# Optimization experiments

Hardware: AMD Instinct MI355X
Metric: run time of the kernel (lower is better)

The kernel has to match this reference:

```python
import jax, jax.numpy as jnp
import numpy as np
import math

B, N, DEG, D = 128, 512, 8, 128
E = B * N * DEG
K1 = math.ceil(0.8 * N)    # 410 nodes kept per graph after pool1
K2 = math.ceil(0.8 * K1)   # 328 nodes kept per graph after pool2


def setup_inputs() -> dict:
    key = jax.random.key(0)
    ks = jax.random.split(key, 24)
    x = jax.random.normal(ks[0], (B * N, D), jnp.float32)
    # random edges within each graph, then offset to global node ids
    src_l = jax.random.randint(ks[1], (B, N * DEG), 0, N)
    dst_l = jax.random.randint(ks[2], (B, N * DEG), 0, N)
    offs = (jnp.arange(B) * N)[:, None]
    edge_index = jnp.stack([(src_l + offs).reshape(-1), (dst_l + offs).reshape(-1)]).astype(jnp.int32)
    w = lambda k, s: (jax.random.normal(k, s, jnp.float32) * 0.05)
    return {
        "x": x, "edge_index": edge_index,
        "W1r": w(ks[3], (D, 128)), "W1n": w(ks[4], (D, 128)), "b1": jnp.zeros((128,), jnp.float32),
        "p1": w(ks[5], (128,)),
        "W2r": w(ks[6], (128, 128)), "W2n": w(ks[7], (128, 128)), "b2": jnp.zeros((128,), jnp.float32),
        "p2": w(ks[8], (128,)),
        "lw1": w(ks[9], (256, 128)), "lb1": jnp.zeros((128,), jnp.float32),
        "lw2": w(ks[10], (128, 64)), "lb2": jnp.zeros((64,), jnp.float32),
        "lw3": w(ks[11], (64, 1)), "lb3": jnp.zeros((1,), jnp.float32),
    }


def _conv(h, src, dst, Wr, Wn, b):
    # GraphConv-style spatio-temporal message passing, sum aggregation
    msg = h[src] @ Wn                                   # [E, 128]
    agg = jax.ops.segment_sum(msg, dst, num_segments=B * N)
    return h @ Wr + agg + b


def _topk_mask(score, k, prev_mask):
    # per-graph top-k node selection (TopKPooling); restrict to prev_mask
    s = jnp.where(prev_mask, score, -jnp.inf).reshape(B, N)
    idx = jax.lax.top_k(s, k)[1]                        # [B, k]
    m = jnp.zeros((B, N), bool).at[jnp.arange(B)[:, None], idx].set(True)
    return m.reshape(B * N)


def _readout(h, mask, k):
    # concat of global max pool and global mean pool over kept nodes
    hm = jnp.where(mask[:, None], h, -jnp.inf).reshape(B, N, -1)
    gmax = hm.max(axis=1)
    gmean = (h * mask[:, None].astype(h.dtype)).reshape(B, N, -1).sum(axis=1) / k
    return jnp.concatenate([gmax, gmean], axis=1)       # [B, 256]


def reference(x, edge_index, W1r, W1n, b1, p1, W2r, W2n, b2, p2, lw1, lb1, lw2, lb2, lw3, lb3):
    src, dst = edge_index[0], edge_index[1]
    # conv1 + relu
    h = jax.nn.relu(_conv(x, src, dst, W1r, W1n, b1))
    # pool1: score = h.p/||p||, keep top-K1, gate by tanh(score)
    s1 = h @ p1 / jnp.linalg.norm(p1)
    m1 = _topk_mask(s1, K1, jnp.ones(B * N, bool))
    h = h * (jnp.tanh(s1) * m1.astype(h.dtype))[:, None]
    x1 = _readout(h, m1, K1)
    # conv2 + relu (dropped nodes have zero features -> zero messages)
    h = jax.nn.relu(_conv(h, src, dst, W2r, W2n, b2))
    s2 = h @ p2 / jnp.linalg.norm(p2)
    m2 = _topk_mask(s2, K2, m1)
    h = h * (jnp.tanh(s2) * m2.astype(h.dtype))[:, None]
    x2 = _readout(h, m2, K2)
    # MLP head (bn1/bn2 are defined but unused in the original forward; dropout is eval-mode identity)
    z = x1 + x2
    z = jax.nn.relu(z @ lw1 + lb1)
    z = jax.nn.relu(z @ lw2 + lb2)
    return jax.nn.sigmoid(z @ lw3 + lb3).squeeze(-1)    # [B]
```

## Files before the change

### kernel.cpp

```cpp
#include <hip/hip_runtime.h>
#include <math.h>

constexpr int B = 128;
constexpr int N = 512;
constexpr int DEG = 8;
constexpr int D = 128;
constexpr int E = B * N * DEG;
constexpr int EPG = N * DEG;
constexpr int NN = B * N;
constexpr int K1 = 410;
constexpr int K2 = 328;
constexpr int PADDEG = 16;

typedef __attribute__((ext_vector_type(8))) short short8;
typedef __attribute__((ext_vector_type(4))) float f32x4;

__device__ __forceinline__ unsigned short f2bf(float f) {
    unsigned int u = __float_as_uint(f);
    unsigned int r = (u + 0x7fffu + ((u >> 16) & 1u)) >> 16;
    return (unsigned short)r;
}
__device__ __forceinline__ float bf2f(unsigned short h) {
    return __uint_as_float(((unsigned int)h) << 16);
}

__global__ __launch_bounds__(256) void k_prepw(const float* __restrict__ W0,
                                               const float* __restrict__ W1,
                                               const float* __restrict__ W2,
                                               const float* __restrict__ W3,
                                               unsigned short* __restrict__ wt) {
    const float* Ws[4] = {W0, W1, W2, W3};
    const int m = blockIdx.x;
    const float* src = Ws[m];
    unsigned short* dH = wt + (size_t)m * 32768;
    unsigned short* dL = dH + 16384;
    for (int idx = threadIdx.x; idx < 16384; idx += 256) {
        int kk = idx >> 7, n = idx & 127;
        float v = src[idx];
        unsigned short h = f2bf(v);
        unsigned short l = f2bf(v - bf2f(h));
        dH[n * 128 + kk] = h;
        dL[n * 128 + kk] = l;
    }
}

__global__ __launch_bounds__(512) void k_csr2(const int* __restrict__ ei,
                                              int* __restrict__ coff,
                                              int* __restrict__ ccnt,
                                              int* __restrict__ csrc,
                                              int* __restrict__ csrcp) {
    __shared__ int cnt[512];
    __shared__ int sa[512];
    __shared__ int offs[512];
    __shared__ int cur[512];
    const int g = blockIdx.x, t = threadIdx.x;
    const int base = g * N;
    const int* srcs = ei + g * EPG;
    const int* dsts = ei + E + g * EPG;
    {
        const int n = base + t;
        int4 self = make_int4(n, n, n, n);
        #pragma unroll
        for (int k4 = 0; k4 < PADDEG / 4; ++k4)
            *(int4*)&csrcp[(size_t)n * PADDEG + k4 * 4] = self;
    }
    cnt[t] = 0;
    __syncthreads();
    #pragma unroll
    for (int e = t; e < EPG; e += 512)
        atomicAdd(&cnt[dsts[e] - base], 1);
    __syncthreads();
    int v = cnt[t];
    sa[t] = v;
    __syncthreads();
    for (int d = 1; d < 512; d <<= 1) {
        int add = (t >= d) ? sa[t - d] : 0;
        __syncthreads();
        sa[t] += add;
        __syncthreads();
    }
    const int excl = sa[t] - v;
    offs[t] = excl;
    cur[t] = excl;
    coff[base + t] = g * EPG + excl;
    ccnt[base + t] = v;
    __syncthreads();
    #pragma unroll
    for (int e = t; e < EPG; e += 512) {
        int d = dsts[e] - base;
        int pos = atomicAdd(&cur[d], 1);
        int s = srcs[e];
        csrc[g * EPG + pos] = s;
        int lpos = pos - offs[d];
        if (lpos < PADDEG) csrcp[(size_t)(base + d) * PADDEG + lpos] = s;
    }
}

__global__ __launch_bounds__(256, 2) void k_gather(const float* __restrict__ feat,
                                                   const float* __restrict__ gate,
                                                   const int* __restrict__ coff,
                                                   const int* __restrict__ ccnt,
                                                   const int* __restrict__ csrc,
                                                   const int* __restrict__ csrcp,
                                                   float* __restrict__ aggout) {
    const int bid = blockIdx.x;
    const int xcd = bid & 7;
    const int j = bid >> 3;
    const int g = ((j & 15) << 3) | xcd;
    const int chunk = j >> 4;
    const int t = threadIdx.x;
    const int lane = t & 31, grp = t >> 5;
    const int fo = lane * 4;
    #pragma unroll
    for (int it = 0; it < 4; ++it) {
        const int n = g * N + chunk * 32 + it * 8 + grp;
        const int deg = ccnt[n];
        int idx[PADDEG];
        *(int4*)&idx[0]  = *(const int4*)&csrcp[(size_t)n * PADDEG + 0];
        *(int4*)&idx[4]  = *(const int4*)&csrcp[(size_t)n * PADDEG + 4];
        *(int4*)&idx[8]  = *(const int4*)&csrcp[(size_t)n * PADDEG + 8];
        *(int4*)&idx[12] = *(const int4*)&csrcp[(size_t)n * PADDEG + 12];
        float4 acc = make_float4(0.f, 0.f, 0.f, 0.f);
        #pragma unroll
        for (int k = 0; k < PADDEG; ++k) {
            if (k < deg) {
                float wk = gate ? gate[idx[k]] : 1.0f;
                float4 v = *(const float4*)&feat[(size_t)idx[k] * D + fo];
                acc.x = fmaf(v.x, wk, acc.x);
                acc.y = fmaf(v.y, wk, acc.y);
                acc.z = fmaf(v.z, wk, acc.z);
                acc.w = fmaf(v.w, wk, acc.w);
            }
        }
        if (deg > PADDEG) {
            const int start = coff[n];
            for (int k = PADDEG; k < deg; ++k) {
                int ix = csrc[start + k];
                float gt = gate ? gate[ix] : 1.0f;
                float4 v = *(const float4*)&feat[(size_t)ix * D + fo];
                acc.x = fmaf(v.x, gt, acc.x);
                acc.y = fmaf(v.y, gt, acc.y);
                acc.z = fmaf(v.z, gt, acc.z);
                acc.w = fmaf(v.w, gt, acc.w);
            }
        }
        *(float4*)&aggout[(size_t)n * D + fo] = acc;
    }
}

__global__ __launch_bounds__(256, 2) void k_gemm(const float* __restrict__ A0,
                                                 const float* __restrict__ gateA,
                                                 const float* __restrict__ A1,
                                                 const unsigned short* __restrict__ W0t,
                                                 const unsigned short* __restrict__ W1t,
                                                 const float* __restrict__ bias,
                                                 const float* __restrict__ pvec,
                                                 float* __restrict__ out,
                                                 float* __restrict__ sun) {
    __shared__ unsigned short AsH[128 * 40], AsL[128 * 40];
    __shared__ unsigned short BsH[128 * 40], BsL[128 * 40];
    __shared__ float red[128 * 33];
    const int t = threadIdx.x;
    const int r0 = blockIdx.x * 128;
    const int w = t >> 6, lane = t & 63;
    const int lr = lane & 15, kg = (lane >> 4) * 8;
    const int wm = (w >> 1) * 64, wn = (w & 1) * 64;
    const int arow = t >> 1, kb = (t & 1) * 16;
    const float ga = gateA ? gateA[r0 + arow] : 1.0f;

    f32x4 acc[4][4];
    #pragma unroll
    for (int mt = 0; mt < 4; ++mt)
        #pragma unroll
        for (int nt = 0; nt < 4; ++nt)
            acc[mt][nt] = (f32x4)(0.f);

    for (int phase = 0; phase < 2; ++phase) {
        const float* Ap = phase ? A1 : A0;
        const unsigned short* WH = phase ? W1t : W0t;
        const unsigned short* WL = WH + 16384;
        const float gmul = phase ? 1.0f : ga;
        for (int c = 0; c < 4; ++c) {
            const int k0 = c * 32;
            __syncthreads();
            #pragma unroll
            for (int i = 0; i < 4; ++i) {
                float4 av = *(const float4*)&Ap[(size_t)(r0 + arow) * D + k0 + kb + i * 4];
                av.x *= gmul; av.y *= gmul; av.z *= gmul; av.w *= gmul;
                unsigned int h0 = f2bf(av.x), h1 = f2bf(av.y), h2 = f2bf(av.z), h3 = f2bf(av.w);
                uint2 ph; ph.x = h0 | (h1 << 16); ph.y = h2 | (h3 << 16);
                *(uint2*)&AsH[arow * 40 + kb + i * 4] = ph;
                unsigned int l0 = f2bf(av.x - bf2f(h0)), l1 = f2bf(av.y - bf2f(h1));
                unsigned int l2 = f2bf(av.z - bf2f(h2)), l3 = f2bf(av.w - bf2f(h3));
                uint2 pl; pl.x = l0 | (l1 << 16); pl.y = l2 | (l3 << 16);
                *(uint2*)&AsL[arow * 40 + kb + i * 4] = pl;
            }
            {
                const int part = t & 3;
                #pragma unroll
                for (int rep = 0; rep < 2; ++rep) {
                    const int n = (t >> 2) + rep * 64;
                    *(int4*)&BsH[n * 40 + part * 8] = *(const int4*)&WH[n * 128 + k0 + part * 8];
                    *(int4*)&BsL[n * 40 + part * 8] = *(const int4*)&WL[n * 128 + k0 + part * 8];
                }
            }
            __syncthreads();
            short8 aH[4], aL[4], bH[4], bL[4];
            #pragma unroll
            for (int mt = 0; mt < 4; ++mt) {
                aH[mt] = *(const short8*)&AsH[(wm + mt * 16 + lr) * 40 + kg];
                aL[mt] = *(const short8*)&AsL[(wm + mt * 16 + lr) * 40 + kg];
            }
            #pragma unroll
            for (int nt = 0; nt < 4; ++nt) {
                bH[nt] = *(const short8*)&BsH[(wn + nt * 16 + lr) * 40 + kg];
                bL[nt] = *(const short8*)&BsL[(wn + nt * 16 + lr) * 40 + kg];
            }
            #pragma unroll
            for (int mt = 0; mt < 4; ++mt)
                #pragma unroll
                for (int nt = 0; nt < 4; ++nt) {
                    acc[mt][nt] = __builtin_amdgcn_mfma_f32_16x16x32_bf16(aH[mt], bH[nt], acc[mt][nt], 0, 0, 0);
                    acc[mt][nt] = __builtin_amdgcn_mfma_f32_16x16x32_bf16(aH[mt], bL[nt], acc[mt][nt], 0, 0, 0);
                    acc[mt][nt] = __builtin_amdgcn_mfma_f32_16x16x32_bf16(aL[mt], bH[nt], acc[mt][nt], 0, 0, 0);
                }
        }
    }
    float bb[4], pv[4];
    #pragma unroll
    for (int nt = 0; nt < 4; ++nt) {
        bb[nt] = bias[wn + nt * 16 + lr];
        pv[nt] = pvec[wn + nt * 16 + lr];
    }
    #pragma unroll
    for (int mt = 0; mt < 4; ++mt) {
        #pragma unroll
        for (int r = 0; r < 4; ++r) {
            const int rowl = wm + mt * 16 + (lane >> 4) * 4 + r;
            const int row = r0 + rowl;
            float part = 0.f;
            #pragma unroll
            for (int nt = 0; nt < 4; ++nt) {
                float v = acc[mt][nt][r] + bb[nt];
                v = fmaxf(v, 0.f);
                out[(size_t)row * D + wn + nt * 16 + lr] = v;
                part = fmaf(v, pv[nt], part);
            }
            red[rowl * 33 + (w & 1) * 16 + lr] = part;
        }
    }
    __syncthreads();
    if (t < 128) {
        float s = 0.f;
        #pragma unroll
        for (int j = 0; j < 32; ++j) s += red[t * 33 + j];
        sun[r0 + t] = s;
    }
}

__global__ __launch_bounds__(1024) void k_topk_readout(const float* __restrict__ sun,
                                                       const float* __restrict__ p,
                                                       const float* __restrict__ prevmask,
                                                       int K, float invK,
                                                       const float* __restrict__ h,
                                                       float* __restrict__ gate,
                                                       float* __restrict__ mask,
                                                       float* __restrict__ xout) {
    __shared__ float ls[512];
    __shared__ float lg[512];
    __shared__ float lm[512];
    __shared__ float red[128];
    __shared__ float smax[16][64];
    __shared__ float ssum[16][64];
    __shared__ float norm_s;
    const int bid = blockIdx.x;
    const int g = bid >> 1, half = bid & 1;
    const int t = threadIdx.x;
    if (t < 512) {
        const int n = g * N + t;
        float s = sun[n];
        if (prevmask && prevmask[n] == 0.0f) s = -INFINITY;
        ls[t] = s;
    }
    if (t < 128) { float pvv = p[t]; red[t] = pvv * pvv; }
    __syncthreads();
    if (t < 64) red[t] += red[t + 64];
    __syncthreads();
    if (t < 32) red[t] += red[t + 32];
    __syncthreads();
    if (t == 0) {
        float s = 0.f;
        #pragma unroll
        for (int i = 0; i < 32; ++i) s += red[i];
        norm_s = sqrtf(s);
    }
    __syncthreads();
    if (t < 512) {
        const float s = ls[t];
        int cnt = 0;
        for (int jj = 0; jj < 512; ++jj) {
            float sj = ls[jj];
            cnt += (sj > s || (sj == s && jj < t)) ? 1 : 0;
        }
        const bool keep = cnt < K;
        const float gv = keep ? tanhf(s / norm_s) : 0.0f;
        const float mv = keep ? 1.0f : 0.0f;
        lg[t] = gv; lm[t] = mv;
        gate[g * N + t] = gv; mask[g * N + t] = mv;
    }
    __syncthreads();
    const int f = half * 64 + (t & 63), sub = t >> 6;
    float vmax = -INFINITY, vsum = 0.f;
    for (int nl = sub; nl < N; nl += 16) {
        const float v = h[(size_t)(g * N + nl) * D + f] * lg[nl];
        vsum += v;
        if (lm[nl] != 0.f) vmax = fmaxf(vmax, v);
    }
    smax[sub][t & 63] = vmax;
    ssum[sub][t & 63] = vsum;
    __syncthreads();
    if (t < 64) {
        float m = smax[0][t], s = ssum[0][t];
        #pragma unroll
        for (int k = 1; k < 16; ++k) { m = fmaxf(m, smax[k][t]); s += ssum[k][t]; }
        xout[g * 256 + half * 64 + t] = m;
        xout[g * 256 + 128 + half * 64 + t] = s * invK;
    }
}

__global__ __launch_bounds__(128) void k_mlp(const float* __restrict__ X1,
                                             const float* __restrict__ X2,
                                             const float* __restrict__ lw1,
                                             const float* __restrict__ lb1,
                                             const float* __restrict__ lw2,
                                             const float* __restrict__ lb2,
                                             const float* __restrict__ lw3,
                                             const float* __restrict__ lb3,
                                             float* __restrict__ out) {
    __shared__ float z[256];
    __shared__ float o1[128];
    __shared__ float o2p[64];
    const int g = blockIdx.x, t = threadIdx.x;
    z[t] = X1[g * 256 + t] + X2[g * 256 + t];
    z[t + 128] = X1[g * 256 + 128 + t] + X2[g * 256 + 128 + t];
    __syncthreads();
    float a = lb1[t];
    for (int i = 0; i < 256; ++i) a = fmaf(z[i], lw1[i * 128 + t], a);
    o1[t] = fmaxf(a, 0.f);
    __syncthreads();
    if (t < 64) {
        float b = lb2[t];
        for (int i = 0; i < 128; ++i) b = fmaf(o1[i], lw2[i * 64 + t], b);
        o2p[t] = fmaxf(b, 0.f) * lw3[t];
    }
    __syncthreads();
    if (t == 0) {
        float sacc = lb3[0];
        for (int i = 0; i < 64; ++i) sacc += o2p[i];
        out[g] = 1.f / (1.f + expf(-sacc));
    }
}

extern "C" void kernel_launch(void* const* d_in, const int* in_sizes, int n_in,
                              void* d_out, int out_size, void* d_ws, size_t ws_size,
                              hipStream_t stream) {
    const float* x    = (const float*)d_in[0];
    const int*   ei   = (const int*)d_in[1];
    const float* W1r  = (const float*)d_in[2];
    const float* W1n  = (const float*)d_in[3];
    const float* b1   = (const float*)d_in[4];
    const float* p1   = (const float*)d_in[5];
    const float* W2r  = (const float*)d_in[6];
    const float* W2n  = (const float*)d_in[7];
    const float* b2   = (const float*)d_in[8];
    const float* p2   = (const float*)d_in[9];
    const float* lw1  = (const float*)d_in[10];
    const float* lb1  = (const float*)d_in[11];
    const float* lw2  = (const float*)d_in[12];
    const float* lb2  = (const float*)d_in[13];
    const float* lw3  = (const float*)d_in[14];
    const float* lb3  = (const float*)d_in[15];
    float* out = (float*)d_out;

    char* w = (char*)d_ws;
    float* h1  = (float*)w; w += (size_t)NN * D * 4;
    float* h2  = (float*)w; w += (size_t)NN * D * 4;
    float* agg = (float*)w; w += (size_t)NN * D * 4;
    int* coff  = (int*)w;   w += (size_t)NN * 4;
    int* ccnt  = (int*)w;   w += (size_t)NN * 4;
    int* csrc  = (int*)w;   w += (size_t)E * 4;
    int* csrcp = (int*)w;   w += (size_t)NN * PADDEG * 4;
    unsigned short* wt = (unsigned short*)w; w += (size_t)4 * 2 * 16384 * 2;
    float* sun = (float*)w; w += (size_t)NN * 4;
    float* g1  = (float*)w; w += (size_t)NN * 4;
    float* m1  = (float*)w; w += (size_t)NN * 4;
    float* g2  = (float*)w; w += (size_t)NN * 4;
    float* m2  = (float*)w; w += (size_t)NN * 4;
    float* X1  = (float*)w; w += (size_t)B * 256 * 4;
    float* X2  = (float*)w; w += (size_t)B * 256 * 4;

    const unsigned short* wt1r = wt;
    const unsigned short* wt1n = wt + 1 * 32768;
    const unsigned short* wt2r = wt + 2 * 32768;
    const unsigned short* wt2n = wt + 3 * 32768;

    k_prepw<<<4, 256, 0, stream>>>(W1r, W1n, W2r, W2n, wt);
    k_csr2<<<B, 512, 0, stream>>>(ei, coff, ccnt, csrc, csrcp);

    k_gather<<<2048, 256, 0, stream>>>(x, nullptr, coff, ccnt, csrc, csrcp, agg);
    k_gemm<<<NN / 128, 256, 0, stream>>>(x, nullptr, agg, wt1r, wt1n, b1, p1, h1, sun);
    k_topk_readout<<<2 * B, 1024, 0, stream>>>(sun, p1, nullptr, K1, 1.0f / (float)K1, h1, g1, m1, X1);

    k_gather<<<2048, 256, 0, stream>>>(h1, g1, coff, ccnt, csrc, csrcp, agg);
    k_gemm<<<NN / 128, 256, 0, stream>>>(h1, g1, agg, wt2r, wt2n, b2, p2, h2, sun);
    k_topk_readout<<<2 * B, 1024, 0, stream>>>(sun, p2, m1, K2, 1.0f / (float)K2, h2, g2, m2, X2);

    k_mlp<<<B, 128, 0, stream>>>(X1, X2, lw1, lb1, lw2, lb2, lw3, lb3, out);
}
```

Before: 300.5 us.

## Fuse neighbor gather into conv GEMM A-tile load and parallelize weight prep

Removes the separate gather kernel and its aggregated-feature buffer: the GEMM now computes the neighbor sum on the fly while staging the second-phase A tile, with block-to-graph mapping chosen to keep a graph's features on one XCD. This avoids writing and re-reading an NN x 128 fp32 intermediate twice per forward. The cost is that the gather now runs with only 512 blocks, one thread per row handling 16 columns, so per-thread latency and register pressure (idx, wk and vals arrays) grow. Weight prep is also spread from 4 blocks to 256 blocks.

```diff
diff --git a/kernel.cpp b/kernel.cpp
--- a/kernel.cpp
+++ b/kernel.cpp
@@ -30,18 +30,17 @@
                                                const float* __restrict__ W3,
                                                unsigned short* __restrict__ wt) {
     const float* Ws[4] = {W0, W1, W2, W3};
-    const int m = blockIdx.x;
+    const int m = blockIdx.x >> 6;
+    const int idx = (blockIdx.x & 63) * 256 + threadIdx.x;
     const float* src = Ws[m];
     unsigned short* dH = wt + (size_t)m * 32768;
     unsigned short* dL = dH + 16384;
-    for (int idx = threadIdx.x; idx < 16384; idx += 256) {
-        int kk = idx >> 7, n = idx & 127;
-        float v = src[idx];
-        unsigned short h = f2bf(v);
-        unsigned short l = f2bf(v - bf2f(h));
-        dH[n * 128 + kk] = h;
-        dL[n * 128 + kk] = l;
-    }
+    int kk = idx >> 7, n = idx & 127;
+    float v = src[idx];
+    unsigned short h = f2bf(v);
+    unsigned short l = f2bf(v - bf2f(h));
+    dH[n * 128 + kk] = h;
+    dL[n * 128 + kk] = l;
 }
 
 __global__ __launch_bounds__(512) void k_csr2(const int* __restrict__ ei,
@@ -96,77 +95,44 @@
     }
 }
 
-__global__ __launch_bounds__(256, 2) void k_gather(const float* __restrict__ feat,
-                                                   const float* __restrict__ gate,
-                                                   const int* __restrict__ coff,
-                                                   const int* __restrict__ ccnt,
-                                                   const int* __restrict__ csrc,
-                                                   const int* __restrict__ csrcp,
-                                                   float* __restrict__ aggout) {
-    const int bid = blockIdx.x;
-    const int xcd = bid & 7;
-    const int j = bid >> 3;
-    const int g = ((j & 15) << 3) | xcd;
-    const int chunk = j >> 4;
-    const int t = threadIdx.x;
-    const int lane = t & 31, grp = t >> 5;
-    const int fo = lane * 4;
-    #pragma unroll
-    for (int it = 0; it < 4; ++it) {
-        const int n = g * N + chunk * 32 + it * 8 + grp;
-        const int deg = ccnt[n];
-        int idx[PADDEG];
-        *(int4*)&idx[0]  = *(const int4*)&csrcp[(size_t)n * PADDEG + 0];
-        *(int4*)&idx[4]  = *(const int4*)&csrcp[(size_t)n * PADDEG + 4];
-        *(int4*)&idx[8]  = *(const int4*)&csrcp[(size_t)n * PADDEG + 8];
-        *(int4*)&idx[12] = *(const int4*)&csrcp[(size_t)n * PADDEG + 12];
-        float4 acc = make_float4(0.f, 0.f, 0.f, 0.f);
-        #pragma unroll
-        for (int k = 0; k < PADDEG; ++k) {
-            if (k < deg) {
-                float wk = gate ? gate[idx[k]] : 1.0f;
-                float4 v = *(const float4*)&feat[(size_t)idx[k] * D + fo];
-                acc.x = fmaf(v.x, wk, acc.x);
-                acc.y = fmaf(v.y, wk, acc.y);
-                acc.z = fmaf(v.z, wk, acc.z);
-                acc.w = fmaf(v.w, wk, acc.w);
-            }
-        }
-        if (deg > PADDEG) {
-            const int start = coff[n];
-            for (int k = PADDEG; k < deg; ++k) {
-                int ix = csrc[start + k];
-                float gt = gate ? gate[ix] : 1.0f;
-                float4 v = *(const float4*)&feat[(size_t)ix * D + fo];
-                acc.x = fmaf(v.x, gt, acc.x);
-                acc.y = fmaf(v.y, gt, acc.y);
-                acc.z = fmaf(v.z, gt, acc.z);
-                acc.w = fmaf(v.w, gt, acc.w);
-            }
-        }
-        *(float4*)&aggout[(size_t)n * D + fo] = acc;
-    }
-}
-
-__global__ __launch_bounds__(256, 2) void k_gemm(const float* __restrict__ A0,
-                                                 const float* __restrict__ gateA,
-                                                 const float* __restrict__ A1,
-                                                 const unsigned short* __restrict__ W0t,
-                                                 const unsigned short* __restrict__ W1t,
-                                                 const float* __restrict__ bias,
-                                                 const float* __restrict__ pvec,
-                                                 float* __restrict__ out,
-                                                 float* __restrict__ sun) {
+__global__ __launch_bounds__(256, 2) void k_fused(const float* __restrict__ feat,
+                                                  const float* __restrict__ gate,
+                                                  const int* __restrict__ coff,
+                                                  const int* __restrict__ ccnt,
+                                                  const int* __restrict__ csrc,
+                                                  const int* __restrict__ csrcp,
+                                                  const unsigned short* __restrict__ W0t,
+                                                  const unsigned short* __restrict__ W1t,
+                                                  const float* __restrict__ bias,
+                                                  const float* __restrict__ pvec,
+                                                  float* __restrict__ out,
+                                                  float* __restrict__ sun) {
     __shared__ unsigned short AsH[128 * 40], AsL[128 * 40];
     __shared__ unsigned short BsH[128 * 40], BsL[128 * 40];
     __shared__ float red[128 * 33];
     const int t = threadIdx.x;
-    const int r0 = blockIdx.x * 128;
+    const int bid = blockIdx.x;
+    const int xcd = bid & 7, j = bid >> 3;
+    const int g = (j & 15) * 8 + xcd;
+    const int chunkRow = j >> 4;
+    const int r0 = g * N + chunkRow * 128;
     const int w = t >> 6, lane = t & 63;
     const int lr = lane & 15, kg = (lane >> 4) * 8;
     const int wm = (w >> 1) * 64, wn = (w & 1) * 64;
     const int arow = t >> 1, kb = (t & 1) * 16;
-    const float ga = gateA ? gateA[r0 + arow] : 1.0f;
+    const int node = r0 + arow;
+
+    const int deg = ccnt[node];
+    const float ga = gate ? gate[node] : 1.0f;
+    int idx[PADDEG];
+    *(int4*)&idx[0]  = *(const int4*)&csrcp[(size_t)node * PADDEG + 0];
+    *(int4*)&idx[4]  = *(const int4*)&csrcp[(size_t)node * PADDEG + 4];
+    *(int4*)&idx[8]  = *(const int4*)&csrcp[(size_t)node * PADDEG + 8];
+    *(int4*)&idx[12] = *(const int4*)&csrcp[(size_t)node * PADDEG + 12];
+    float wk[PADDEG];
+    #pragma unroll
+    for (int nb = 0; nb < PADDEG; ++nb)
+        wk[nb] = (nb < deg) ? (gate ? gate[idx[nb]] : 1.0f) : 0.0f;
 
     f32x4 acc[4][4];
     #pragma unroll
@@ -176,25 +142,68 @@
             acc[mt][nt] = (f32x4)(0.f);
 
     for (int phase = 0; phase < 2; ++phase) {
-        const float* Ap = phase ? A1 : A0;
         const unsigned short* WH = phase ? W1t : W0t;
         const unsigned short* WL = WH + 16384;
-        const float gmul = phase ? 1.0f : ga;
         for (int c = 0; c < 4; ++c) {
             const int k0 = c * 32;
             __syncthreads();
+            float vals[16];
+            if (phase == 0) {
+                const float* fp = &feat[(size_t)node * D + k0 + kb];
+                #pragma unroll
+                for (int i = 0; i < 4; ++i) {
+                    float4 v = ((const float4*)fp)[i];
+                    vals[i * 4 + 0] = v.x * ga; vals[i * 4 + 1] = v.y * ga;
+                    vals[i * 4 + 2] = v.z * ga; vals[i * 4 + 3] = v.w * ga;
+                }
+            } else {
+                #pragma unroll
+                for (int i = 0; i < 16; ++i) vals[i] = 0.f;
+                #pragma unroll
+                for (int nb = 0; nb < PADDEG; ++nb) {
+                    if (nb < deg) {
+                        const float* fp = &feat[(size_t)idx[nb] * D + k0 + kb];
+                        const float wn_ = wk[nb];
+                        #pragma unroll
+                        for (int i = 0; i < 4; ++i) {
+                            float4 v = ((const float4*)fp)[i];
+                            vals[i * 4 + 0] = fmaf(v.x, wn_, vals[i * 4 + 0]);
+                            vals[i * 4 + 1] = fmaf(v.y, wn_, vals[i * 4 + 1]);
+                            vals[i * 4 + 2] = fmaf(v.z, wn_, vals[i * 4 + 2]);
+                            vals[i * 4 + 3] = fmaf(v.w, wn_, vals[i * 4 + 3]);
+                        }
+                    }
+                }
+                if (deg > PADDEG) {
+                    const int start = coff[node];
+                    for (int k = PADDEG; k < deg; ++k) {
+                        int ix = csrc[start + k];
+                        float gt = gate ? gate[ix] : 1.0f;
+                        const float* fp = &feat[(size_t)ix * D + k0 + kb];
+                        #pragma unroll
+                        for (int i = 0; i < 4; ++i) {
+                            float4 v = ((const float4*)fp)[i];
+                            vals[i * 4 + 0] = fmaf(v.x, gt, vals[i * 4 + 0]);
+                            vals[i * 4 + 1] = fmaf(v.y, gt, vals[i * 4 + 1]);
+                            vals[i * 4 + 2] = fmaf(v.z, gt, vals[i * 4 + 2]);
+                            vals[i * 4 + 3] = fmaf(v.w, gt, vals[i * 4 + 3]);
+                        }
+                    }
+                }
+            }
+            unsigned int ph[8], pl[8];
             #pragma unroll
-            for (int i = 0; i < 4; ++i) {
-                float4 av = *(const float4*)&Ap[(size_t)(r0 + arow) * D + k0 + kb + i * 4];
-                av.x *= gmul; av.y *= gmul; av.z *= gmul; av.w *= gmul;
-                unsigned int h0 = f2bf(av.x), h1 = f2bf(av.y), h2 = f2bf(av.z), h3 = f2bf(av.w);
-                uint2 ph; ph.x = h0 | (h1 << 16); ph.y = h2 | (h3 << 16);
-                *(uint2*)&AsH[arow * 40 + kb + i * 4] = ph;
-                unsigned int l0 = f2bf(av.x - bf2f(h0)), l1 = f2bf(av.y - bf2f(h1));
-                unsigned int l2 = f2bf(av.z - bf2f(h2)), l3 = f2bf(av.w - bf2f(h3));
-                uint2 pl; pl.x = l0 | (l1 << 16); pl.y = l2 | (l3 << 16);
-                *(uint2*)&AsL[arow * 40 + kb + i * 4] = pl;
-            }
+            for (int jj = 0; jj < 8; ++jj) {
+                unsigned int h0 = f2bf(vals[2 * jj]), h1 = f2bf(vals[2 * jj + 1]);
+                ph[jj] = h0 | (h1 << 16);
+                unsigned int l0 = f2bf(vals[2 * jj] - bf2f((unsigned short)h0));
+                unsigned int l1 = f2bf(vals[2 * jj + 1] - bf2f((unsigned short)h1));
+                pl[jj] = l0 | (l1 << 16);
+            }
+            *(int4*)&AsH[arow * 40 + kb]     = make_int4(ph[0], ph[1], ph[2], ph[3]);
+            *(int4*)&AsH[arow * 40 + kb + 8] = make_int4(ph[4], ph[5], ph[6], ph[7]);
+            *(int4*)&AsL[arow * 40 + kb]     = make_int4(pl[0], pl[1], pl[2], pl[3]);
+            *(int4*)&AsL[arow * 40 + kb + 8] = make_int4(pl[4], pl[5], pl[6], pl[7]);
             {
                 const int part = t & 3;
                 #pragma unroll
@@ -253,7 +262,7 @@
     if (t < 128) {
         float s = 0.f;
         #pragma unroll
-        for (int j = 0; j < 32; ++j) s += red[t * 33 + j];
+        for (int jj = 0; jj < 32; ++jj) s += red[t * 33 + jj];
         sun[r0 + t] = s;
     }
 }
@@ -385,7 +394,6 @@
     char* w = (char*)d_ws;
     float* h1  = (float*)w; w += (size_t)NN * D * 4;
     float* h2  = (float*)w; w += (size_t)NN * D * 4;
-    float* agg = (float*)w; w += (size_t)NN * D * 4;
     int* coff  = (int*)w;   w += (size_t)NN * 4;
     int* ccnt  = (int*)w;   w += (size_t)NN * 4;
     int* csrc  = (int*)w;   w += (size_t)E * 4;
@@ -404,15 +412,15 @@
     const unsigned short* wt2r = wt + 2 * 32768;
     const unsigned short* wt2n = wt + 3 * 32768;
 
-    k_prepw<<<4, 256, 0, stream>>>(W1r, W1n, W2r, W2n, wt);
+    k_prepw<<<256, 256, 0, stream>>>(W1r, W1n, W2r, W2n, wt);
     k_csr2<<<B, 512, 0, stream>>>(ei, coff, ccnt, csrc, csrcp);
 
-    k_gather<<<2048, 256, 0, stream>>>(x, nullptr, coff, ccnt, csrc, csrcp, agg);
-    k_gemm<<<NN / 128, 256, 0, stream>>>(x, nullptr, agg, wt1r, wt1n, b1, p1, h1, sun);
+    k_fused<<<NN / 128, 256, 0, stream>>>(x, nullptr, coff, ccnt, csrc, csrcp,
+                                          wt1r, wt1n, b1, p1, h1, sun);
     k_topk_readout<<<2 * B, 1024, 0, stream>>>(sun, p1, nullptr, K1, 1.0f / (float)K1, h1, g1, m1, X1);
 
-    k_gather<<<2048, 256, 0, stream>>>(h1, g1, coff, ccnt, csrc, csrcp, agg);
-    k_gemm<<<NN / 128, 256, 0, stream>>>(h1, g1, agg, wt2r, wt2n, b2, p2, h2, sun);
+    k_fused<<<NN / 128, 256, 0, stream>>>(h1, g1, coff, ccnt, csrc, csrcp,
+                                          wt2r, wt2n, b2, p2, h2, sun);
     k_topk_readout<<<2 * B, 1024, 0, stream>>>(sun, p2, m1, K2, 1.0f / (float)K2, h2, g2, m2, X2);
 
     k_mlp<<<B, 128, 0, stream>>>(X1, X2, lw1, lb1, lw2, lb2, lw3, lb3, out);
```

Result: slower. 520.3 us (+73.2%).

## Rebuild CSR with deterministic per-node shared-memory scan; parallelize weight prep

Applied to the files above, without the earlier changes.

The CSR build kernel now stages each graph's edges in shared memory. Each thread linearly scans all edges for its own destination node, replacing the atomic counting and scatter passes, and the full csrc list is written only for nodes with more than PADDEG neighbours. Each thread now does an O(EPG) serial scan of shared memory, which may cost more than the atomics it replaces, and a single block uses roughly 55KB of shared memory. Weight conversion now runs as 256 blocks with one element per thread instead of 4 looping blocks.

```diff
diff --git a/kernel.cpp b/kernel.cpp
--- a/kernel.cpp
+++ b/kernel.cpp
@@ -30,18 +30,17 @@
                                                const float* __restrict__ W3,
                                                unsigned short* __restrict__ wt) {
     const float* Ws[4] = {W0, W1, W2, W3};
-    const int m = blockIdx.x;
+    const int m = blockIdx.x >> 6;
+    const int idx = (blockIdx.x & 63) * 256 + threadIdx.x;
     const float* src = Ws[m];
     unsigned short* dH = wt + (size_t)m * 32768;
     unsigned short* dL = dH + 16384;
-    for (int idx = threadIdx.x; idx < 16384; idx += 256) {
-        int kk = idx >> 7, n = idx & 127;
-        float v = src[idx];
-        unsigned short h = f2bf(v);
-        unsigned short l = f2bf(v - bf2f(h));
-        dH[n * 128 + kk] = h;
-        dL[n * 128 + kk] = l;
-    }
+    int kk = idx >> 7, n = idx & 127;
+    float v = src[idx];
+    unsigned short h = f2bf(v);
+    unsigned short l = f2bf(v - bf2f(h));
+    dH[n * 128 + kk] = h;
+    dL[n * 128 + kk] = l;
 }
 
 __global__ __launch_bounds__(512) void k_csr2(const int* __restrict__ ei,
@@ -49,29 +48,30 @@
                                               int* __restrict__ ccnt,
                                               int* __restrict__ csrc,
                                               int* __restrict__ csrcp) {
-    __shared__ int cnt[512];
+    __shared__ int lsrc[EPG];
+    __shared__ unsigned short ldst[EPG];
+    __shared__ int lnb[PADDEG * 512];
     __shared__ int sa[512];
-    __shared__ int offs[512];
-    __shared__ int cur[512];
     const int g = blockIdx.x, t = threadIdx.x;
     const int base = g * N;
+    const int node = base + t;
     const int* srcs = ei + g * EPG;
     const int* dsts = ei + E + g * EPG;
-    {
-        const int n = base + t;
-        int4 self = make_int4(n, n, n, n);
-        #pragma unroll
-        for (int k4 = 0; k4 < PADDEG / 4; ++k4)
-            *(int4*)&csrcp[(size_t)n * PADDEG + k4 * 4] = self;
-    }
-    cnt[t] = 0;
-    __syncthreads();
-    #pragma unroll
-    for (int e = t; e < EPG; e += 512)
-        atomicAdd(&cnt[dsts[e] - base], 1);
-    __syncthreads();
-    int v = cnt[t];
-    sa[t] = v;
+    for (int e = t; e < EPG; e += 512) {
+        lsrc[e] = srcs[e];
+        ldst[e] = (unsigned short)(dsts[e] - base);
+    }
+    #pragma unroll
+    for (int i = 0; i < PADDEG; ++i) lnb[i * 512 + t] = node;
+    __syncthreads();
+    int lp = 0;
+    for (int e = 0; e < EPG; ++e) {
+        if ((int)ldst[e] == t) {
+            if (lp < PADDEG) lnb[lp * 512 + t] = lsrc[e];
+            ++lp;
+        }
+    }
+    sa[t] = lp;
     __syncthreads();
     for (int d = 1; d < 512; d <<= 1) {
         int add = (t >= d) ? sa[t - d] : 0;
@@ -79,20 +79,20 @@
         sa[t] += add;
         __syncthreads();
     }
-    const int excl = sa[t] - v;
-    offs[t] = excl;
-    cur[t] = excl;
-    coff[base + t] = g * EPG + excl;
-    ccnt[base + t] = v;
-    __syncthreads();
-    #pragma unroll
-    for (int e = t; e < EPG; e += 512) {
-        int d = dsts[e] - base;
-        int pos = atomicAdd(&cur[d], 1);
-        int s = srcs[e];
-        csrc[g * EPG + pos] = s;
-        int lpos = pos - offs[d];
-        if (lpos < PADDEG) csrcp[(size_t)(base + d) * PADDEG + lpos] = s;
+    const int excl = sa[t] - lp;
+    coff[node] = g * EPG + excl;
+    ccnt[node] = lp;
+    #pragma unroll
+    for (int j = 0; j < PADDEG / 4; ++j) {
+        int4 v = make_int4(lnb[(4 * j + 0) * 512 + t], lnb[(4 * j + 1) * 512 + t],
+                           lnb[(4 * j + 2) * 512 + t], lnb[(4 * j + 3) * 512 + t]);
+        *(int4*)&csrcp[(size_t)node * PADDEG + 4 * j] = v;
+    }
+    if (lp > PADDEG) {
+        int pos = g * EPG + excl;
+        for (int e = 0; e < EPG; ++e) {
+            if ((int)ldst[e] == t) csrc[pos++] = lsrc[e];
+        }
     }
 }
 
@@ -404,7 +404,7 @@
     const unsigned short* wt2r = wt + 2 * 32768;
     const unsigned short* wt2n = wt + 3 * 32768;
 
-    k_prepw<<<4, 256, 0, stream>>>(W1r, W1n, W2r, W2n, wt);
+    k_prepw<<<256, 256, 0, stream>>>(W1r, W1n, W2r, W2n, wt);
     k_csr2<<<B, 512, 0, stream>>>(ei, coff, ccnt, csrc, csrcp);
 
     k_gather<<<2048, 256, 0, stream>>>(x, nullptr, coff, ccnt, csrc, csrcp, agg);
```

Measured after the change: 723.0 us. 2.41x slower.

## Parallelize weight prep and sort per-node neighbor lists in CSR build

Applied to the files above, without the earlier changes.

The weight-conversion kernel now runs 256 blocks, one element per thread, where it used to loop inside 4 blocks. The CSR build stages the padded neighbor list in shared memory and writes it out with vectorized stores. It also insertion-sorts each node's source indices, so gathers touch memory in ascending order with better locality. The cost is extra serial sorting work per thread, including a global-memory sort for nodes with high degree, which could lengthen the CSR kernel.

```diff
diff --git a/kernel.cpp b/kernel.cpp
--- a/kernel.cpp
+++ b/kernel.cpp
@@ -30,18 +30,17 @@
                                                const float* __restrict__ W3,
                                                unsigned short* __restrict__ wt) {
     const float* Ws[4] = {W0, W1, W2, W3};
-    const int m = blockIdx.x;
+    const int m = blockIdx.x >> 6;
+    const int idx = (blockIdx.x & 63) * 256 + threadIdx.x;
     const float* src = Ws[m];
     unsigned short* dH = wt + (size_t)m * 32768;
     unsigned short* dL = dH + 16384;
-    for (int idx = threadIdx.x; idx < 16384; idx += 256) {
-        int kk = idx >> 7, n = idx & 127;
-        float v = src[idx];
-        unsigned short h = f2bf(v);
-        unsigned short l = f2bf(v - bf2f(h));
-        dH[n * 128 + kk] = h;
-        dL[n * 128 + kk] = l;
-    }
+    int kk = idx >> 7, n = idx & 127;
+    float v = src[idx];
+    unsigned short h = f2bf(v);
+    unsigned short l = f2bf(v - bf2f(h));
+    dH[n * 128 + kk] = h;
+    dL[n * 128 + kk] = l;
 }
 
 __global__ __launch_bounds__(512) void k_csr2(const int* __restrict__ ei,
@@ -53,18 +52,15 @@
     __shared__ int sa[512];
     __shared__ int offs[512];
     __shared__ int cur[512];
+    __shared__ int lnb[PADDEG * 512];
     const int g = blockIdx.x, t = threadIdx.x;
     const int base = g * N;
+    const int node = base + t;
     const int* srcs = ei + g * EPG;
     const int* dsts = ei + E + g * EPG;
-    {
-        const int n = base + t;
-        int4 self = make_int4(n, n, n, n);
-        #pragma unroll
-        for (int k4 = 0; k4 < PADDEG / 4; ++k4)
-            *(int4*)&csrcp[(size_t)n * PADDEG + k4 * 4] = self;
-    }
     cnt[t] = 0;
+    #pragma unroll
+    for (int i = 0; i < PADDEG; ++i) lnb[i * 512 + t] = node;
     __syncthreads();
     #pragma unroll
     for (int e = t; e < EPG; e += 512)
@@ -82,8 +78,8 @@
     const int excl = sa[t] - v;
     offs[t] = excl;
     cur[t] = excl;
-    coff[base + t] = g * EPG + excl;
-    ccnt[base + t] = v;
+    coff[node] = g * EPG + excl;
+    ccnt[node] = v;
     __syncthreads();
     #pragma unroll
     for (int e = t; e < EPG; e += 512) {
@@ -92,7 +88,39 @@
         int s = srcs[e];
         csrc[g * EPG + pos] = s;
         int lpos = pos - offs[d];
-        if (lpos < PADDEG) csrcp[(size_t)(base + d) * PADDEG + lpos] = s;
+        if (lpos < PADDEG) lnb[lpos * 512 + d] = s;
+    }
+    __syncthreads();
+    const int deg = v;
+    if (deg <= PADDEG) {
+        for (int i = 1; i < deg; ++i) {
+            int key = lnb[i * 512 + t];
+            int j = i - 1;
+            while (j >= 0 && lnb[j * 512 + t] > key) {
+                lnb[(j + 1) * 512 + t] = lnb[j * 512 + t];
+                --j;
+            }
+            lnb[(j + 1) * 512 + t] = key;
+        }
+    } else {
+        const int start = g * EPG + excl;
+        for (int i = 1; i < deg; ++i) {
+            int key = csrc[start + i];
+            int j = i - 1;
+            while (j >= 0 && csrc[start + j] > key) {
+                csrc[start + j + 1] = csrc[start + j];
+                --j;
+            }
+            csrc[start + j + 1] = key;
+        }
+        #pragma unroll
+        for (int i = 0; i < PADDEG; ++i) lnb[i * 512 + t] = csrc[start + i];
+    }
+    #pragma unroll
+    for (int j = 0; j < PADDEG / 4; ++j) {
+        int4 vv = make_int4(lnb[(4 * j + 0) * 512 + t], lnb[(4 * j + 1) * 512 + t],
+                            lnb[(4 * j + 2) * 512 + t], lnb[(4 * j + 3) * 512 + t]);
+        *(int4*)&csrcp[(size_t)node * PADDEG + 4 * j] = vv;
     }
 }
 
@@ -404,7 +432,7 @@
     const unsigned short* wt2r = wt + 2 * 32768;
     const unsigned short* wt2n = wt + 3 * 32768;
 
-    k_prepw<<<4, 256, 0, stream>>>(W1r, W1n, W2r, W2n, wt);
+    k_prepw<<<256, 256, 0, stream>>>(W1r, W1n, W2r, W2n, wt);
     k_csr2<<<B, 512, 0, stream>>>(ei, coff, ccnt, csrc, csrcp);
 
     k_gather<<<2048, 256, 0, stream>>>(x, nullptr, coff, ccnt, csrc, csrcp, agg);
```

Measured after the change: 305.6 us. About the same (+1.7%).
